# Kernel optimization log

Measured on AMD Instinct MI355X. Metric: run time of the kernel, lower is better.

Reference implementation:

```python
import jax, jax.numpy as jnp
import numpy as np

# Canonical topology: root object with K arrays, each array has L number leaves.
# Weights are tied across paths (tie_weights_containers=tie_weights_primitives=True),
# NumberEmbedder runs in eval mode with initial buffers mean=0, sqmean=1 -> identity norm.

K, L, D = 8192, 128, 64


def setup_inputs() -> dict:
    key = jax.random.key(0)
    ks = jax.random.split(key, 16)
    s = 1.0 / np.sqrt(D)
    return {
        "x": jax.random.normal(ks[0], (K, L), dtype=jnp.float32),
        "W_num": jax.random.normal(ks[1], (D, 1), dtype=jnp.float32) * s,
        "b_num": jax.random.normal(ks[2], (D,), dtype=jnp.float32) * s,
        "W_ih": jax.random.normal(ks[3], (4 * D, 2 * D), dtype=jnp.float32) * s,
        "W_hh": jax.random.normal(ks[4], (4 * D, D), dtype=jnp.float32) * s,
        "b_ih": jax.random.normal(ks[5], (4 * D,), dtype=jnp.float32) * s,
        "b_hh": jax.random.normal(ks[6], (4 * D,), dtype=jnp.float32) * s,
        "W_aout": jax.random.normal(ks[7], (D, D), dtype=jnp.float32) * s,
        "b_aout": jax.random.normal(ks[8], (D,), dtype=jnp.float32) * s,
        "W_fh": jax.random.normal(ks[9], (D, D), dtype=jnp.float32) * s,
        "b_fh": jax.random.normal(ks[10], (D,), dtype=jnp.float32) * s,
        "W_iouh": jax.random.normal(ks[11], (3 * D, D), dtype=jnp.float32) * s,
        "b_iouh": jax.random.normal(ks[12], (3 * D,), dtype=jnp.float32) * s,
        "W_oout": jax.random.normal(ks[13], (D, D), dtype=jnp.float32) * s,
        "b_oout": jax.random.normal(ks[14], (D,), dtype=jnp.float32) * s,
    }


def _forward(x, W_num, b_num, W_ih, W_hh, b_ih, b_hh, W_aout, b_aout,
             W_fh, b_fh, W_iouh, b_iouh, W_oout, b_oout):
    d = W_hh.shape[1]
    # --- NumberEmbedder: Linear(1, d) on identity-normalized numbers; c = 0 ---
    emb = x[..., None] * W_num[:, 0] + b_num          # [K, L, d]
    xs = jnp.transpose(emb, (1, 0, 2))                # [L, K, d] time-major for scan
    # --- ArrayEmbedder: LSTMCell over children; input = cat(child_h, child_c) ---
    # child_c is identically zero, so only the first half of W_ih contributes.
    W_ih_h = W_ih[:, :d]                              # [4d, d]
    bias = b_ih + b_hh                                # [4d]

    def step(carry, x_t):
        h, c = carry
        gates = x_t @ W_ih_h.T + h @ W_hh.T + bias    # [K, 4d]
        i, f, g, o = jnp.split(gates, 4, axis=1)
        c2 = jax.nn.sigmoid(f) * c + jax.nn.sigmoid(i) * jnp.tanh(g)
        h2 = jax.nn.sigmoid(o) * jnp.tanh(c2)
        return (h2, c2), None

    h0 = jnp.zeros((x.shape[0], d), dtype=x.dtype)
    (h_arr, c_arr), _ = jax.lax.scan(step, (h0, h0), xs)
    h_hat = h_arr @ W_aout.T + b_aout                 # [K, d] array lout
    # --- ObjectEmbedder: child-sum TreeLSTM over the K array states ---
    f = h_hat @ W_fh.T + b_fh                         # [K, d]
    fc_sum = jnp.sum(jax.nn.sigmoid(f) * c_arr, axis=0, keepdims=True)  # [1, d]
    hs_bar = jnp.sum(h_hat, axis=0, keepdims=True)    # [1, d]
    iou = hs_bar @ W_iouh.T + b_iouh                  # [1, 3d]
    i, o, u = jnp.split(iou, 3, axis=1)
    c_obj = jax.nn.sigmoid(i) * jnp.tanh(u) + fc_sum
    h_obj = jax.nn.sigmoid(o) * jnp.tanh(c_obj)
    h_hat_obj = h_obj @ W_oout.T + b_oout             # [1, d] object lout
    # root forward returns cat(h, c)
    return jnp.concatenate([h_hat_obj, c_obj], axis=1)  # [1, 2d]


def reference(x, W_num, b_num, W_ih, W_hh, b_ih, b_hh, W_aout, b_aout,
              W_fh, b_fh, W_iouh, b_iouh, W_oout, b_oout):
    return _forward(x, W_num, b_num, W_ih, W_hh, b_ih, b_hh, W_aout, b_aout,
                    W_fh, b_fh, W_iouh, b_iouh, W_oout, b_oout)
```

## Files before the change

### kernel.cpp

```cpp
#include <hip/hip_runtime.h>
#include <cstddef>

#define D  64
#define L  128
#define NT 256
#define ROWS 16
#define XS_STRIDE 129
#define HBS 72
#define KROWS 8192

typedef __attribute__((ext_vector_type(8))) short short8;
typedef __attribute__((ext_vector_type(4))) float floatx4;

__device__ __forceinline__ float fast_rcp(float x) {
#if defined(__has_builtin)
#if __has_builtin(__builtin_amdgcn_rcpf)
  return __builtin_amdgcn_rcpf(x);
#else
  return 1.0f / x;
#endif
#else
  return 1.0f / x;
#endif
}
__device__ __forceinline__ float sigf(float x) {
  return fast_rcp(1.0f + __expf(-x));
}
__device__ __forceinline__ float tanh_fast(float x) {
  return 2.0f * fast_rcp(1.0f + __expf(-2.0f * x)) - 1.0f;
}
__device__ __forceinline__ unsigned short f2bf_rtne(float f) {
  unsigned int u = __float_as_uint(f);
  u += 0x7fffu + ((u >> 16) & 1u);
  return (unsigned short)(u >> 16);
}
__device__ __forceinline__ float bf2f(unsigned short s) {
  return __uint_as_float(((unsigned int)s) << 16);
}

__global__ __launch_bounds__(NT, 2)
void lstm_main(const float* __restrict__ x,
               const float* __restrict__ W_num,
               const float* __restrict__ b_num,
               const float* __restrict__ W_ih,
               const float* __restrict__ W_hh,
               const float* __restrict__ b_ih,
               const float* __restrict__ b_hh,
               const float* __restrict__ W_aout,
               const float* __restrict__ b_aout,
               const float* __restrict__ W_fh,
               const float* __restrict__ b_fh,
               float* __restrict__ acc_out)
{
  __shared__ __align__(16) float xs[ROWS * XS_STRIDE];
  __shared__ __align__(16) short hb_hi[2][ROWS * HBS];
  __shared__ __align__(16) short hb_lo[2][ROWS * HBS];

  const int tid  = threadIdx.x;
  const int w    = tid >> 6;
  const int lane = tid & 63;
  const int quad = lane >> 4;
  const int c16  = lane & 15;
  const int k0   = blockIdx.x * ROWS;
  const int dcol = w * 16 + c16;

  for (int i = tid; i < ROWS * (L / 4); i += NT) {
    int r = i >> 5, c4 = i & 31;
    float4 v = ((const float4*)(x + (size_t)(k0 + r) * L))[c4];
    float* dst = &xs[r * XS_STRIDE + c4 * 4];
    dst[0] = v.x; dst[1] = v.y; dst[2] = v.z; dst[3] = v.w;
  }
  for (int i = tid; i < ROWS * HBS; i += NT) { hb_hi[0][i] = 0; hb_lo[0][i] = 0; }

  float An[4], Bc[4];
#pragma unroll
  for (int g = 0; g < 4; ++g) {
    int j = g * 64 + dcol;
    float a = 0.0f, b = b_ih[j] + b_hh[j];
    for (int e = 0; e < D; ++e) {
      float wih = W_ih[(size_t)j * (2 * D) + e];
      a = fmaf(W_num[e], wih, a);
      b = fmaf(b_num[e], wih, b);
    }
    An[g] = a; Bc[g] = b;
  }

  short8 Bhi[4][2], Blo[4][2];
#pragma unroll
  for (int g = 0; g < 4; ++g) {
#pragma unroll
    for (int kk = 0; kk < 2; ++kk) {
      const float* wp = W_hh + (size_t)(g * 64 + dcol) * D + kk * 32 + quad * 8;
      short8 hi8, lo8;
#pragma unroll
      for (int j = 0; j < 8; ++j) {
        float v = wp[j];
        unsigned short h = f2bf_rtne(v);
        hi8[j] = (short)h;
        lo8[j] = (short)f2bf_rtne(v - bf2f(h));
      }
      Bhi[g][kk] = hi8; Blo[g][kk] = lo8;
    }
  }

  float creg[4] = {0.f, 0.f, 0.f, 0.f};
  float hreg[4] = {0.f, 0.f, 0.f, 0.f};
  __syncthreads();

  int p = 0;
  for (int t = 0; t < L; ++t) {
    short8 ahi[2], alo[2];
#pragma unroll
    for (int kk = 0; kk < 2; ++kk) {
      int off = c16 * HBS + kk * 32 + quad * 8;
      ahi[kk] = *(const short8*)&hb_hi[p][off];
      alo[kk] = *(const short8*)&hb_lo[p][off];
    }
    float xv[4];
#pragma unroll
    for (int r = 0; r < 4; ++r) xv[r] = xs[(quad * 4 + r) * XS_STRIDE + t];
    floatx4 acc[4];
#pragma unroll
    for (int g = 0; g < 4; ++g)
      acc[g] = (floatx4){fmaf(An[g], xv[0], Bc[g]), fmaf(An[g], xv[1], Bc[g]),
                         fmaf(An[g], xv[2], Bc[g]), fmaf(An[g], xv[3], Bc[g])};
#pragma unroll
    for (int kk = 0; kk < 2; ++kk) {
#pragma unroll
      for (int g = 0; g < 4; ++g) {
        acc[g] = __builtin_amdgcn_mfma_f32_16x16x32_bf16(ahi[kk], Bhi[g][kk], acc[g], 0, 0, 0);
        acc[g] = __builtin_amdgcn_mfma_f32_16x16x32_bf16(alo[kk], Bhi[g][kk], acc[g], 0, 0, 0);
        acc[g] = __builtin_amdgcn_mfma_f32_16x16x32_bf16(ahi[kk], Blo[g][kk], acc[g], 0, 0, 0);
      }
    }
#pragma unroll
    for (int r = 0; r < 4; ++r) {
      float gi = acc[0][r], gf = acc[1][r], gg = acc[2][r], go = acc[3][r];
      float c2 = sigf(gf) * creg[r] + sigf(gi) * tanh_fast(gg);
      float h2 = sigf(go) * tanh_fast(c2);
      creg[r] = c2;
      hreg[r] = h2;
      unsigned int u = __float_as_uint(h2);
      unsigned short hi = (unsigned short)(u >> 16);
      float hif = __uint_as_float(u & 0xffff0000u);
      unsigned short lo = (unsigned short)(__float_as_uint(h2 - hif) >> 16);
      int row = quad * 4 + r;
      hb_hi[p ^ 1][row * HBS + dcol] = (short)hi;
      hb_lo[p ^ 1][row * HBS + dcol] = (short)lo;
    }
    __syncthreads();
    p ^= 1;
  }

#pragma unroll
  for (int r = 0; r < 4; ++r) xs[(quad * 4 + r) * XS_STRIDE + dcol] = hreg[r];
  __syncthreads();

  float hhat[4];
#pragma unroll
  for (int r = 0; r < 4; ++r) {
    float a = b_aout[dcol];
    const float4* wa = (const float4*)(W_aout + (size_t)dcol * D);
    const float* hp = &xs[(quad * 4 + r) * XS_STRIDE];
#pragma unroll
    for (int e4 = 0; e4 < 16; ++e4) {
      float4 wv = wa[e4];
      a = fmaf(wv.x, hp[e4 * 4 + 0], a);
      a = fmaf(wv.y, hp[e4 * 4 + 1], a);
      a = fmaf(wv.z, hp[e4 * 4 + 2], a);
      a = fmaf(wv.w, hp[e4 * 4 + 3], a);
    }
    hhat[r] = a;
  }
  __syncthreads();
#pragma unroll
  for (int r = 0; r < 4; ++r) xs[(quad * 4 + r) * XS_STRIDE + 64 + dcol] = hhat[r];
  __syncthreads();

  float pfc = 0.0f, phs = 0.0f;
#pragma unroll
  for (int r = 0; r < 4; ++r) {
    float f = b_fh[dcol];
    const float4* wf = (const float4*)(W_fh + (size_t)dcol * D);
    const float* hp = &xs[(quad * 4 + r) * XS_STRIDE + 64];
#pragma unroll
    for (int e4 = 0; e4 < 16; ++e4) {
      float4 wv = wf[e4];
      f = fmaf(wv.x, hp[e4 * 4 + 0], f);
      f = fmaf(wv.y, hp[e4 * 4 + 1], f);
      f = fmaf(wv.z, hp[e4 * 4 + 2], f);
      f = fmaf(wv.w, hp[e4 * 4 + 3], f);
    }
    pfc = fmaf(sigf(f), creg[r], pfc);
    phs += hhat[r];
  }
  pfc += __shfl_xor(pfc, 16); pfc += __shfl_xor(pfc, 32);
  phs += __shfl_xor(phs, 16); phs += __shfl_xor(phs, 32);
  if (quad == 0) {
    atomicAdd(acc_out + dcol, pfc);
    atomicAdd(acc_out + D + dcol, phs);
  }
}

__global__ void lstm_final(const float* __restrict__ acc,
                           const float* __restrict__ W_iouh,
                           const float* __restrict__ b_iouh,
                           const float* __restrict__ W_oout,
                           const float* __restrict__ b_oout,
                           float* __restrict__ out)
{
  __shared__ float hobj[D];
  __shared__ float cobj[D];
  const int d = threadIdx.x;
  float vi = b_iouh[d], vo = b_iouh[D + d], vu = b_iouh[2 * D + d];
  for (int e = 0; e < D; ++e) {
    float hs = acc[D + e];
    vi = fmaf(W_iouh[(size_t)d * D + e],           hs, vi);
    vo = fmaf(W_iouh[(size_t)(D + d) * D + e],     hs, vo);
    vu = fmaf(W_iouh[(size_t)(2 * D + d) * D + e], hs, vu);
  }
  float c_obj = sigf(vi) * tanh_fast(vu) + acc[d];
  float h_obj = sigf(vo) * tanh_fast(c_obj);
  hobj[d] = h_obj;
  cobj[d] = c_obj;
  __syncthreads();
  float hh = b_oout[d];
  for (int e = 0; e < D; ++e) hh = fmaf(W_oout[(size_t)d * D + e], hobj[e], hh);
  out[d]     = hh;
  out[D + d] = cobj[d];
}

extern "C" void kernel_launch(void* const* d_in, const int* in_sizes, int n_in,
                              void* d_out, int out_size, void* d_ws, size_t ws_size,
                              hipStream_t stream) {
  const float* x      = (const float*)d_in[0];
  const float* W_num  = (const float*)d_in[1];
  const float* b_num  = (const float*)d_in[2];
  const float* W_ih   = (const float*)d_in[3];
  const float* W_hh   = (const float*)d_in[4];
  const float* b_ih   = (const float*)d_in[5];
  const float* b_hh   = (const float*)d_in[6];
  const float* W_aout = (const float*)d_in[7];
  const float* b_aout = (const float*)d_in[8];
  const float* W_fh   = (const float*)d_in[9];
  const float* b_fh   = (const float*)d_in[10];
  const float* W_iouh = (const float*)d_in[11];
  const float* b_iouh = (const float*)d_in[12];
  const float* W_oout = (const float*)d_in[13];
  const float* b_oout = (const float*)d_in[14];
  float* acc = (float*)d_ws;
  float* out = (float*)d_out;

  hipMemsetAsync(d_ws, 0, 2 * D * sizeof(float), stream);
  lstm_main<<<KROWS / ROWS, NT, 0, stream>>>(x, W_num, b_num, W_ih, W_hh, b_ih, b_hh,
                                             W_aout, b_aout, W_fh, b_fh, acc);
  lstm_final<<<1, D, 0, stream>>>(acc, W_iouh, b_iouh, W_oout, b_oout, out);
}
```

Before: 241.6 us.

## Process two row tiles per block, fold gate scaling into weights, fuse final kernel

Each block now handles 32 rows as two independent 16-row MFMA chains interleaved per timestep, so the grid drops to 256 blocks at one block per SIMD-set. The interleaving is meant to hide MFMA and transcendental latency inside the serial recurrence. Gate pre-activations are prescaled by -log2e (or -2log2e for the tanh gate) inside the weights and biases, so activations use exp2 directly. The separate final kernel is folded in through a last-block-done atomic counter, which removes one launch. The cost is halved grid parallelism (256 blocks on 256 CUs), higher register pressure, and rounding of the scaled weights into the bf16 hi/lo split.

```diff
diff --git a/kernel.cpp b/kernel.cpp
--- a/kernel.cpp
+++ b/kernel.cpp
@@ -1,13 +1,14 @@
 #include <hip/hip_runtime.h>
 #include <cstddef>
 
-#define D  64
-#define L  128
-#define NT 256
-#define ROWS 16
-#define XS_STRIDE 129
+#define D   64
+#define L   128
+#define NT  256
+#define ROWS 32
+#define XSS 129
 #define HBS 72
-#define KROWS 8192
+#define NBLK 256
+#define LOG2E 1.4426950408889634f
 
 typedef __attribute__((ext_vector_type(8))) short short8;
 typedef __attribute__((ext_vector_type(4))) float floatx4;
@@ -23,11 +24,14 @@
   return 1.0f / x;
 #endif
 }
-__device__ __forceinline__ float sigf(float x) {
-  return fast_rcp(1.0f + __expf(-x));
-}
-__device__ __forceinline__ float tanh_fast(float x) {
-  return 2.0f * fast_rcp(1.0f + __expf(-2.0f * x)) - 1.0f;
+__device__ __forceinline__ float sig2(float G) {
+  return fast_rcp(1.0f + __builtin_exp2f(G));
+}
+__device__ __forceinline__ float tanh2(float G) {
+  return fmaf(2.0f, fast_rcp(1.0f + __builtin_exp2f(G)), -1.0f);
+}
+__device__ __forceinline__ float sig_plain(float x) {
+  return fast_rcp(1.0f + __builtin_exp2f(-LOG2E * x));
 }
 __device__ __forceinline__ unsigned short f2bf_rtne(float f) {
   unsigned int u = __float_as_uint(f);
@@ -37,8 +41,14 @@
 __device__ __forceinline__ float bf2f(unsigned short s) {
   return __uint_as_float(((unsigned int)s) << 16);
 }
-
-__global__ __launch_bounds__(NT, 2)
+__device__ __forceinline__ void pack_split(float h2, short* hi, short* lo) {
+  unsigned int u = __float_as_uint(h2);
+  *hi = (short)(u >> 16);
+  float hif = __uint_as_float(u & 0xffff0000u);
+  *lo = (short)((unsigned short)(__float_as_uint(h2 - hif) >> 16));
+}
+
+__global__ __launch_bounds__(NT, 1)
 void lstm_main(const float* __restrict__ x,
                const float* __restrict__ W_num,
                const float* __restrict__ b_num,
@@ -50,11 +60,21 @@
                const float* __restrict__ b_aout,
                const float* __restrict__ W_fh,
                const float* __restrict__ b_fh,
-               float* __restrict__ acc_out)
+               const float* __restrict__ W_iouh,
+               const float* __restrict__ b_iouh,
+               const float* __restrict__ W_oout,
+               const float* __restrict__ b_oout,
+               float* __restrict__ acc_out,
+               float* __restrict__ out)
 {
-  __shared__ __align__(16) float xs[ROWS * XS_STRIDE];
-  __shared__ __align__(16) short hb_hi[2][ROWS * HBS];
-  __shared__ __align__(16) short hb_lo[2][ROWS * HBS];
+  __shared__ __align__(16) float xs[ROWS * XSS];
+  __shared__ __align__(16) short hA_hi[2][16 * HBS];
+  __shared__ __align__(16) short hA_lo[2][16 * HBS];
+  __shared__ __align__(16) short hB_hi[2][16 * HBS];
+  __shared__ __align__(16) short hB_lo[2][16 * HBS];
+  __shared__ float sacc[2 * D];
+  __shared__ float hobj[D];
+  __shared__ int   is_last;
 
   const int tid  = threadIdx.x;
   const int w    = tid >> 6;
@@ -67,10 +87,14 @@
   for (int i = tid; i < ROWS * (L / 4); i += NT) {
     int r = i >> 5, c4 = i & 31;
     float4 v = ((const float4*)(x + (size_t)(k0 + r) * L))[c4];
-    float* dst = &xs[r * XS_STRIDE + c4 * 4];
+    float* dst = &xs[r * XSS + c4 * 4];
     dst[0] = v.x; dst[1] = v.y; dst[2] = v.z; dst[3] = v.w;
   }
-  for (int i = tid; i < ROWS * HBS; i += NT) { hb_hi[0][i] = 0; hb_lo[0][i] = 0; }
+  for (int i = tid; i < 16 * HBS; i += NT) {
+    hA_hi[0][i] = 0; hA_lo[0][i] = 0; hB_hi[0][i] = 0; hB_lo[0][i] = 0;
+  }
+
+  const float gscale[4] = {-LOG2E, -LOG2E, -2.0f * LOG2E, -LOG2E};
 
   float An[4], Bc[4];
 #pragma unroll
@@ -82,7 +106,7 @@
       a = fmaf(W_num[e], wih, a);
       b = fmaf(b_num[e], wih, b);
     }
-    An[g] = a; Bc[g] = b;
+    An[g] = a * gscale[g]; Bc[g] = b * gscale[g];
   }
 
   short8 Bhi[4][2], Blo[4][2];
@@ -94,7 +118,7 @@
       short8 hi8, lo8;
 #pragma unroll
       for (int j = 0; j < 8; ++j) {
-        float v = wp[j];
+        float v = wp[j] * gscale[g];
         unsigned short h = f2bf_rtne(v);
         hi8[j] = (short)h;
         lo8[j] = (short)f2bf_rtne(v - bf2f(h));
@@ -103,96 +127,113 @@
     }
   }
 
-  float creg[4] = {0.f, 0.f, 0.f, 0.f};
-  float hreg[4] = {0.f, 0.f, 0.f, 0.f};
+  float cA[4] = {0.f,0.f,0.f,0.f}, cB[4] = {0.f,0.f,0.f,0.f};
+  float hAr[4] = {0.f,0.f,0.f,0.f}, hBr[4] = {0.f,0.f,0.f,0.f};
   __syncthreads();
 
   int p = 0;
   for (int t = 0; t < L; ++t) {
-    short8 ahi[2], alo[2];
+    short8 ahiA[2], aloA[2], ahiB[2], aloB[2];
 #pragma unroll
     for (int kk = 0; kk < 2; ++kk) {
       int off = c16 * HBS + kk * 32 + quad * 8;
-      ahi[kk] = *(const short8*)&hb_hi[p][off];
-      alo[kk] = *(const short8*)&hb_lo[p][off];
-    }
-    float xv[4];
-#pragma unroll
-    for (int r = 0; r < 4; ++r) xv[r] = xs[(quad * 4 + r) * XS_STRIDE + t];
-    floatx4 acc[4];
-#pragma unroll
-    for (int g = 0; g < 4; ++g)
-      acc[g] = (floatx4){fmaf(An[g], xv[0], Bc[g]), fmaf(An[g], xv[1], Bc[g]),
-                         fmaf(An[g], xv[2], Bc[g]), fmaf(An[g], xv[3], Bc[g])};
+      ahiA[kk] = *(const short8*)&hA_hi[p][off];
+      aloA[kk] = *(const short8*)&hA_lo[p][off];
+      ahiB[kk] = *(const short8*)&hB_hi[p][off];
+      aloB[kk] = *(const short8*)&hB_lo[p][off];
+    }
+    float xvA[4], xvB[4];
+#pragma unroll
+    for (int r = 0; r < 4; ++r) {
+      xvA[r] = xs[(quad * 4 + r) * XSS + t];
+      xvB[r] = xs[(16 + quad * 4 + r) * XSS + t];
+    }
+    floatx4 aA[4], aB[4];
+#pragma unroll
+    for (int g = 0; g < 4; ++g) {
+      aA[g] = (floatx4){fmaf(An[g], xvA[0], Bc[g]), fmaf(An[g], xvA[1], Bc[g]),
+                        fmaf(An[g], xvA[2], Bc[g]), fmaf(An[g], xvA[3], Bc[g])};
+      aB[g] = (floatx4){fmaf(An[g], xvB[0], Bc[g]), fmaf(An[g], xvB[1], Bc[g]),
+                        fmaf(An[g], xvB[2], Bc[g]), fmaf(An[g], xvB[3], Bc[g])};
+    }
 #pragma unroll
     for (int kk = 0; kk < 2; ++kk) {
 #pragma unroll
       for (int g = 0; g < 4; ++g) {
-        acc[g] = __builtin_amdgcn_mfma_f32_16x16x32_bf16(ahi[kk], Bhi[g][kk], acc[g], 0, 0, 0);
-        acc[g] = __builtin_amdgcn_mfma_f32_16x16x32_bf16(alo[kk], Bhi[g][kk], acc[g], 0, 0, 0);
-        acc[g] = __builtin_amdgcn_mfma_f32_16x16x32_bf16(ahi[kk], Blo[g][kk], acc[g], 0, 0, 0);
+        aA[g] = __builtin_amdgcn_mfma_f32_16x16x32_bf16(ahiA[kk], Bhi[g][kk], aA[g], 0, 0, 0);
+        aB[g] = __builtin_amdgcn_mfma_f32_16x16x32_bf16(ahiB[kk], Bhi[g][kk], aB[g], 0, 0, 0);
+        aA[g] = __builtin_amdgcn_mfma_f32_16x16x32_bf16(aloA[kk], Bhi[g][kk], aA[g], 0, 0, 0);
+        aB[g] = __builtin_amdgcn_mfma_f32_16x16x32_bf16(aloB[kk], Bhi[g][kk], aB[g], 0, 0, 0);
+        aA[g] = __builtin_amdgcn_mfma_f32_16x16x32_bf16(ahiA[kk], Blo[g][kk], aA[g], 0, 0, 0);
+        aB[g] = __builtin_amdgcn_mfma_f32_16x16x32_bf16(ahiB[kk], Blo[g][kk], aB[g], 0, 0, 0);
       }
     }
 #pragma unroll
     for (int r = 0; r < 4; ++r) {
-      float gi = acc[0][r], gf = acc[1][r], gg = acc[2][r], go = acc[3][r];
-      float c2 = sigf(gf) * creg[r] + sigf(gi) * tanh_fast(gg);
-      float h2 = sigf(go) * tanh_fast(c2);
-      creg[r] = c2;
-      hreg[r] = h2;
-      unsigned int u = __float_as_uint(h2);
-      unsigned short hi = (unsigned short)(u >> 16);
-      float hif = __uint_as_float(u & 0xffff0000u);
-      unsigned short lo = (unsigned short)(__float_as_uint(h2 - hif) >> 16);
       int row = quad * 4 + r;
-      hb_hi[p ^ 1][row * HBS + dcol] = (short)hi;
-      hb_lo[p ^ 1][row * HBS + dcol] = (short)lo;
+      float c2a = sig2(aA[1][r]) * cA[r] + sig2(aA[0][r]) * tanh2(aA[2][r]);
+      float c2b = sig2(aB[1][r]) * cB[r] + sig2(aB[0][r]) * tanh2(aB[2][r]);
+      float h2a = sig2(aA[3][r]) * tanh2(-2.0f * LOG2E * c2a);
+      float h2b = sig2(aB[3][r]) * tanh2(-2.0f * LOG2E * c2b);
+      cA[r] = c2a; cB[r] = c2b; hAr[r] = h2a; hBr[r] = h2b;
+      short hi, lo;
+      pack_split(h2a, &hi, &lo);
+      hA_hi[p ^ 1][row * HBS + dcol] = hi;
+      hA_lo[p ^ 1][row * HBS + dcol] = lo;
+      pack_split(h2b, &hi, &lo);
+      hB_hi[p ^ 1][row * HBS + dcol] = hi;
+      hB_lo[p ^ 1][row * HBS + dcol] = lo;
     }
     __syncthreads();
     p ^= 1;
   }
 
 #pragma unroll
-  for (int r = 0; r < 4; ++r) xs[(quad * 4 + r) * XS_STRIDE + dcol] = hreg[r];
-  __syncthreads();
-
-  float hhat[4];
-#pragma unroll
   for (int r = 0; r < 4; ++r) {
+    xs[(quad * 4 + r) * XSS + dcol]        = hAr[r];
+    xs[(16 + quad * 4 + r) * XSS + dcol]   = hBr[r];
+  }
+  __syncthreads();
+
+  float hhat[8];
+#pragma unroll
+  for (int q = 0; q < 8; ++q) {
+    int row = (q & 1) * 16 + quad * 4 + (q >> 1);
     float a = b_aout[dcol];
     const float4* wa = (const float4*)(W_aout + (size_t)dcol * D);
-    const float* hp = &xs[(quad * 4 + r) * XS_STRIDE];
+    const float* hp = &xs[row * XSS];
 #pragma unroll
     for (int e4 = 0; e4 < 16; ++e4) {
       float4 wv = wa[e4];
-      a = fmaf(wv.x, hp[e4 * 4 + 0], a);
-      a = fmaf(wv.y, hp[e4 * 4 + 1], a);
-      a = fmaf(wv.z, hp[e4 * 4 + 2], a);
-      a = fmaf(wv.w, hp[e4 * 4 + 3], a);
-    }
-    hhat[r] = a;
-  }
-  __syncthreads();
-#pragma unroll
-  for (int r = 0; r < 4; ++r) xs[(quad * 4 + r) * XS_STRIDE + 64 + dcol] = hhat[r];
+      a = fmaf(wv.x, hp[e4*4+0], a); a = fmaf(wv.y, hp[e4*4+1], a);
+      a = fmaf(wv.z, hp[e4*4+2], a); a = fmaf(wv.w, hp[e4*4+3], a);
+    }
+    hhat[q] = a;
+  }
+  __syncthreads();
+#pragma unroll
+  for (int q = 0; q < 8; ++q) {
+    int row = (q & 1) * 16 + quad * 4 + (q >> 1);
+    xs[row * XSS + 64 + dcol] = hhat[q];
+  }
   __syncthreads();
 
   float pfc = 0.0f, phs = 0.0f;
 #pragma unroll
-  for (int r = 0; r < 4; ++r) {
+  for (int q = 0; q < 8; ++q) {
+    int row = (q & 1) * 16 + quad * 4 + (q >> 1);
     float f = b_fh[dcol];
     const float4* wf = (const float4*)(W_fh + (size_t)dcol * D);
-    const float* hp = &xs[(quad * 4 + r) * XS_STRIDE + 64];
+    const float* hp = &xs[row * XSS + 64];
 #pragma unroll
     for (int e4 = 0; e4 < 16; ++e4) {
       float4 wv = wf[e4];
-      f = fmaf(wv.x, hp[e4 * 4 + 0], f);
-      f = fmaf(wv.y, hp[e4 * 4 + 1], f);
-      f = fmaf(wv.z, hp[e4 * 4 + 2], f);
-      f = fmaf(wv.w, hp[e4 * 4 + 3], f);
-    }
-    pfc = fmaf(sigf(f), creg[r], pfc);
-    phs += hhat[r];
+      f = fmaf(wv.x, hp[e4*4+0], f); f = fmaf(wv.y, hp[e4*4+1], f);
+      f = fmaf(wv.z, hp[e4*4+2], f); f = fmaf(wv.w, hp[e4*4+3], f);
+    }
+    float cc = (q & 1) ? cB[q >> 1] : cA[q >> 1];
+    pfc = fmaf(sig_plain(f), cc, pfc);
+    phs += hhat[q];
   }
   pfc += __shfl_xor(pfc, 16); pfc += __shfl_xor(pfc, 32);
   phs += __shfl_xor(phs, 16); phs += __shfl_xor(phs, 32);
@@ -200,34 +241,40 @@
     atomicAdd(acc_out + dcol, pfc);
     atomicAdd(acc_out + D + dcol, phs);
   }
-}
-
-__global__ void lstm_final(const float* __restrict__ acc,
-                           const float* __restrict__ W_iouh,
-                           const float* __restrict__ b_iouh,
-                           const float* __restrict__ W_oout,
-                           const float* __restrict__ b_oout,
-                           float* __restrict__ out)
-{
-  __shared__ float hobj[D];
-  __shared__ float cobj[D];
-  const int d = threadIdx.x;
-  float vi = b_iouh[d], vo = b_iouh[D + d], vu = b_iouh[2 * D + d];
-  for (int e = 0; e < D; ++e) {
-    float hs = acc[D + e];
-    vi = fmaf(W_iouh[(size_t)d * D + e],           hs, vi);
-    vo = fmaf(W_iouh[(size_t)(D + d) * D + e],     hs, vo);
-    vu = fmaf(W_iouh[(size_t)(2 * D + d) * D + e], hs, vu);
-  }
-  float c_obj = sigf(vi) * tanh_fast(vu) + acc[d];
-  float h_obj = sigf(vo) * tanh_fast(c_obj);
-  hobj[d] = h_obj;
-  cobj[d] = c_obj;
-  __syncthreads();
-  float hh = b_oout[d];
-  for (int e = 0; e < D; ++e) hh = fmaf(W_oout[(size_t)d * D + e], hobj[e], hh);
-  out[d]     = hh;
-  out[D + d] = cobj[d];
+
+  __threadfence();
+  if (tid == 0) {
+    unsigned int prev = __hip_atomic_fetch_add((unsigned int*)(acc_out + 2 * D), 1u,
+                                               __ATOMIC_ACQ_REL, __HIP_MEMORY_SCOPE_AGENT);
+    is_last = (prev == NBLK - 1) ? 1 : 0;
+  }
+  __syncthreads();
+  if (!is_last) return;
+  __threadfence();
+  if (tid < 2 * D)
+    sacc[tid] = __hip_atomic_load(acc_out + tid, __ATOMIC_RELAXED, __HIP_MEMORY_SCOPE_AGENT);
+  __syncthreads();
+  if (tid < D) {
+    const int d = tid;
+    float vi = b_iouh[d], vo = b_iouh[D + d], vu = b_iouh[2 * D + d];
+    for (int e = 0; e < D; ++e) {
+      float hs = sacc[D + e];
+      vi = fmaf(W_iouh[(size_t)d * D + e],           hs, vi);
+      vo = fmaf(W_iouh[(size_t)(D + d) * D + e],     hs, vo);
+      vu = fmaf(W_iouh[(size_t)(2 * D + d) * D + e], hs, vu);
+    }
+    float c_obj = sig_plain(vi) * tanh2(-2.0f * LOG2E * vu) + sacc[d];
+    float h_obj = sig_plain(vo) * tanh2(-2.0f * LOG2E * c_obj);
+    hobj[d] = h_obj;
+    out[D + d] = c_obj;
+  }
+  __syncthreads();
+  if (tid < D) {
+    const int d = tid;
+    float hh = b_oout[d];
+    for (int e = 0; e < D; ++e) hh = fmaf(W_oout[(size_t)d * D + e], hobj[e], hh);
+    out[d] = hh;
+  }
 }
 
 extern "C" void kernel_launch(void* const* d_in, const int* in_sizes, int n_in,
@@ -251,8 +298,8 @@
   float* acc = (float*)d_ws;
   float* out = (float*)d_out;
 
-  hipMemsetAsync(d_ws, 0, 2 * D * sizeof(float), stream);
-  lstm_main<<<KROWS / ROWS, NT, 0, stream>>>(x, W_num, b_num, W_ih, W_hh, b_ih, b_hh,
-                                             W_aout, b_aout, W_fh, b_fh, acc);
-  lstm_final<<<1, D, 0, stream>>>(acc, W_iouh, b_iouh, W_oout, b_oout, out);
-}
+  hipMemsetAsync(d_ws, 0, (2 * D + 1) * sizeof(float), stream);
+  lstm_main<<<NBLK, NT, 0, stream>>>(x, W_num, b_num, W_ih, W_hh, b_ih, b_hh,
+                                     W_aout, b_aout, W_fh, b_fh,
+                                     W_iouh, b_iouh, W_oout, b_oout, acc, out);
+}
```

New measurement: 323.9 us. 1.34x slower.
